# Optimization experiments

Measured on AMD Instinct MI355X. Metric: run time of the kernel, lower is better.

The kernel has to match this reference:

```python
import jax, jax.numpy as jnp
import numpy as np

CLIP_LENGTH = 256.0
NUM_CLASSES = 21
OVERLAP_THRESH = 0.5
GAMMA = 2.0
ALPHA = 0.25
EPS = float(np.finfo(np.float32).eps)

B, K, N_GT = 32, 32768, 32


def setup_inputs() -> dict:
    key = jax.random.key(0)
    ks = jax.random.split(key, 9)
    loc_data = jax.random.uniform(ks[0], (B, K, 2), jnp.float32) * 64.0 + 1.0  # frame-unit offsets
    conf_data = jax.random.normal(ks[1], (B, K, NUM_CLASSES), jnp.float32)
    prop_loc_data = jax.random.normal(ks[2], (B, K, 2), jnp.float32)
    prop_conf_data = jax.random.normal(ks[3], (B, K, NUM_CLASSES), jnp.float32)
    center_data = jax.random.normal(ks[4], (B, K, 1), jnp.float32)
    priors = jax.random.uniform(ks[5], (K, 1), jnp.float32)  # normalized centers in [0,1]
    t0 = jax.random.uniform(ks[6], (B, N_GT), jnp.float32) * 0.8
    dur = jax.random.uniform(ks[7], (B, N_GT), jnp.float32) * 0.18 + 0.02
    t1 = jnp.minimum(t0 + dur, 1.0)
    labels = jax.random.randint(ks[8], (B, N_GT), 1, NUM_CLASSES).astype(jnp.float32)
    targets = jnp.stack([t0, t1, labels], axis=-1)  # [B, N, 3]
    return {"loc_data": loc_data, "conf_data": conf_data, "prop_loc_data": prop_loc_data,
            "prop_conf_data": prop_conf_data, "center_data": center_data,
            "priors": priors, "targets": targets}


def _calc_iou(pred, target):
    pl, pr = pred[..., 0], pred[..., 1]
    tl, tr = target[..., 0], target[..., 1]
    inter = jnp.minimum(pl, tl) + jnp.minimum(pr, tr)
    union = (pl + pr) + (tl + tr) - inter
    return inter / jnp.maximum(union, EPS)


def _giou_loss(pred, target):
    pl, pr = pred[..., 0], pred[..., 1]
    tl, tr = target[..., 0], target[..., 1]
    inter = jnp.minimum(pl, tl) + jnp.minimum(pr, tr)
    union = (pl + pr) + (tl + tr) - inter
    ious = inter / jnp.maximum(union, EPS)
    ac = jnp.maximum(pl, tl) + jnp.maximum(pr, tr)
    gious = ious - (ac - union) / jnp.maximum(ac, EPS)
    return 1.0 - gious


_ALPHA_VEC = jnp.full((NUM_CLASSES,), 1.0 - ALPHA, jnp.float32).at[0].set(ALPHA)


def _focal_sum(logits, tgt):
    # FocalLoss_Ori with pre-softmax inside MultiSegmentLoss; reduction=sum
    probs = jax.nn.softmax(logits, axis=-1)
    pt = jnp.take_along_axis(probs, tgt[..., None], axis=-1)[..., 0] + 1e-10
    return (-_ALPHA_VEC[tgt] * (1.0 - pt) ** GAMMA * jnp.log(pt)).sum()


def _match_targets(loc_data_ng, priors, targets):
    # everything here mirrors the torch.no_grad() matching block
    truths = targets[..., :2]                       # [B,N,2]
    labels = targets[..., 2].astype(jnp.int32)      # [B,N]
    center = priors[:, 0]                           # [K]
    left = (center[None, :, None] - truths[:, None, :, 0]) * CLIP_LENGTH   # [B,K,N]
    right = (truths[:, None, :, 1] - center[None, :, None]) * CLIP_LENGTH  # [B,K,N]
    maxn = CLIP_LENGTH * 2.0
    area = jnp.where((left < 0) | (right < 0), maxn, left + right)
    best_area = area.min(-1)                        # [B,K]
    best_idx = area.argmin(-1)                      # [B,K]
    t0 = jnp.take_along_axis(truths[..., 0], best_idx, axis=1)
    t1 = jnp.take_along_axis(truths[..., 1], best_idx, axis=1)
    loc_t = jnp.stack([(center[None, :] - t0) * CLIP_LENGTH,
                       (t1 - center[None, :]) * CLIP_LENGTH], axis=-1)     # [B,K,2]
    conf_t = jnp.take_along_axis(labels, best_idx, axis=1)
    conf_t = jnp.where(best_area >= maxn, 0, conf_t)                       # [B,K]
    iou = _calc_iou(loc_data_ng, loc_t)
    prop_conf_t = jnp.where(iou < OVERLAP_THRESH, 0, conf_t)
    prop_w = loc_data_ng[..., 0] + loc_data_ng[..., 1]
    prop_loc_t = (loc_t - loc_data_ng) / (0.5 * prop_w[..., None])
    return loc_t, conf_t, prop_loc_t, prop_conf_t


def reference(loc_data, conf_data, prop_loc_data, prop_conf_data, center_data, priors, targets):
    loc_t, conf_t, prop_loc_t, prop_conf_t = _match_targets(
        jax.lax.stop_gradient(loc_data), priors, targets)

    pos = conf_t > 0
    posf = pos.astype(loc_data.dtype)
    N = jnp.maximum(posf.sum(), 1.0)
    prop_pos = prop_conf_t > 0
    ppf = prop_pos.astype(loc_data.dtype)
    PN = jnp.maximum(ppf.sum(), 1.0)

    # GIoU localization loss over positives
    loss_l = (_giou_loss(loc_data, loc_t) * posf).sum() / N

    # L1 proposal refinement loss over proposal positives
    loss_prop_l = (jnp.abs(prop_loc_data - prop_loc_t).sum(-1) * ppf).sum() / PN

    # centerness BCE-with-logits against refined IoU, over positives
    prop_pre_w = loc_data[..., 0:1] + loc_data[..., 1:2]
    cur_loc_p = 0.5 * prop_pre_w * prop_loc_data + loc_data
    ious_ct = jnp.maximum(_calc_iou(cur_loc_p, loc_t), 0.0)
    x = center_data[..., 0]
    bce = jnp.maximum(x, 0.0) - x * ious_ct + jnp.log1p(jnp.exp(-jnp.abs(x)))
    loss_ct = (bce * posf).sum() / N

    # focal classification losses over all anchors
    loss_c = _focal_sum(conf_data, conf_t) / N
    loss_prop_c = _focal_sum(prop_conf_data, prop_conf_t) / PN

    return (loss_l, loss_c, loss_prop_l, loss_prop_c, loss_ct)
```

## Files before the change

kernel.cpp:

```cpp
#include <hip/hip_runtime.h>
#include <math.h>

#define NCLS 21
#define NGT 32
#define CLIPLEN 256.0f
#define MAXN 512.0f
#define FEPS 1.1920928955078125e-07f

#define ROWF 21
#define WCH (64 * ROWF)


__device__ __forceinline__ void glds16(const float* g, float* l) {
    __builtin_amdgcn_global_load_lds(
        (const __attribute__((address_space(1))) void*)g,
        (__attribute__((address_space(3))) void*)l, 16, 0, 0);
}
__device__ __forceinline__ void glds4(const float* g, float* l) {
    __builtin_amdgcn_global_load_lds(
        (const __attribute__((address_space(1))) void*)g,
        (__attribute__((address_space(3))) void*)l, 4, 0, 0);
}

__device__ __forceinline__ float focal_term_lds(const float* __restrict__ row, int tgt) {
    float r[NCLS];
#pragma unroll
    for (int i = 0; i < NCLS; ++i) r[i] = row[i];
    float m = r[0];
#pragma unroll
    for (int i = 1; i < NCLS; ++i) m = fmaxf(m, r[i]);
    float s = 0.0f;
    float tl = 0.0f;
#pragma unroll
    for (int i = 0; i < NCLS; ++i) {
        s += __expf(r[i] - m);
        if (i == tgt) tl = r[i];
    }
    float lse = m + __logf(s);
    float pt = __expf(tl - lse) + 1e-10f;
    float a = (tgt == 0) ? 0.25f : 0.75f;
    float om = 1.0f - pt;
    return -a * om * om * __logf(pt);
}

template <bool PARTIALS>
__global__ __launch_bounds__(256) void msl_main(
    const float* __restrict__ loc_data,
    const float* __restrict__ conf_data,
    const float* __restrict__ prop_loc_data,
    const float* __restrict__ prop_conf_data,
    const float* __restrict__ center_data,
    const float* __restrict__ priors,
    const float* __restrict__ targets,
    double* __restrict__ ws,
    int K, int nblk)
{
    __shared__ float s_cls[2][4 * WCH];
    __shared__ float s_t0[NGT], s_t1[NGT], s_lb[NGT];
    __shared__ float s_red[7 * 4];

    const int b    = blockIdx.y;
    const int tid  = threadIdx.x;
    const int lane = tid & 63;
    const int w    = tid >> 6;
    const int kblk = blockIdx.x * 256;
    const int k    = kblk + tid;
    const size_t idx = (size_t)b * K + k;

    if (tid < NGT) {
        const float* tg = targets + ((size_t)b * NGT + tid) * 3;
        s_t0[tid] = tg[0];
        s_t1[tid] = tg[1];
        s_lb[tid] = tg[2];
    }

    {
        const size_t chunk0 = ((size_t)b * K + kblk + w * 64) * ROWF;
        const float* gc = conf_data + chunk0;
        const float* gp = prop_conf_data + chunk0;
        float* lc = &s_cls[0][w * WCH];
        float* lp = &s_cls[1][w * WCH];
#pragma unroll
        for (int i = 0; i < 5; ++i)
            glds16(gc + i * 256 + lane * 4, lc + i * 256);
        glds4(gc + 1280 + lane, lc + 1280);
#pragma unroll
        for (int i = 0; i < 5; ++i)
            glds16(gp + i * 256 + lane * 4, lp + i * 256);
        glds4(gp + 1280 + lane, lp + 1280);
    }

    const float2 loc = ((const float2*)loc_data)[idx];
    const float2 plo = ((const float2*)prop_loc_data)[idx];
    const float  x   = center_data[idx];
    const float  c   = priors[k];

    __syncthreads();

    float bestA = 3.0e38f;
    int bestN = 0;
#pragma unroll
    for (int n = 0; n < NGT; ++n) {
        float l = (c - s_t0[n]) * CLIPLEN;
        float r = (s_t1[n] - c) * CLIPLEN;
        float a = (l < 0.0f || r < 0.0f) ? MAXN : (l + r);
        if (a < bestA) { bestA = a; bestN = n; }
    }
    const float t0 = s_t0[bestN];
    const float t1 = s_t1[bestN];
    const float tl = (c - t0) * CLIPLEN;
    const float tr = (t1 - c) * CLIPLEN;
    int conf_t = (bestA >= MAXN) ? 0 : (int)s_lb[bestN];

    const float pl = loc.x, pr = loc.y;

    const float inter = fminf(pl, tl) + fminf(pr, tr);
    const float uni   = pl + pr + tl + tr - inter;
    const float iou   = inter / fmaxf(uni, FEPS);

    const int prop_conf_t = (iou < 0.5f) ? 0 : conf_t;
    const float posf = (conf_t > 0) ? 1.0f : 0.0f;
    const float ppf  = (prop_conf_t > 0) ? 1.0f : 0.0f;

    const float ac   = fmaxf(pl, tl) + fmaxf(pr, tr);
    const float giou = iou - (ac - uni) / fmaxf(ac, FEPS);
    const float v_ll = (1.0f - giou) * posf;

    const float prop_w = pl + pr;
    const float inv_hw = 1.0f / (0.5f * prop_w);
    const float plt0 = (tl - pl) * inv_hw;
    const float plt1 = (tr - pr) * inv_hw;
    const float v_lpl = (fabsf(plo.x - plt0) + fabsf(plo.y - plt1)) * ppf;

    const float cur0 = 0.5f * prop_w * plo.x + pl;
    const float cur1 = 0.5f * prop_w * plo.y + pr;
    const float in2  = fminf(cur0, tl) + fminf(cur1, tr);
    const float un2  = cur0 + cur1 + tl + tr - in2;
    const float iou2 = fmaxf(in2 / fmaxf(un2, FEPS), 0.0f);
    const float bce  = fmaxf(x, 0.0f) - x * iou2 + log1pf(__expf(-fabsf(x)));
    const float v_ct = bce * posf;

    asm volatile("s_waitcnt vmcnt(0)" ::: "memory");
    const float* rowc = &s_cls[0][w * WCH + lane * ROWF];
    const float* rowp = &s_cls[1][w * WCH + lane * ROWF];
    const float v_lc  = focal_term_lds(rowc, conf_t);
    const float v_lpc = focal_term_lds(rowp, prop_conf_t);

    float vals[7] = { v_ll, v_lc, v_lpl, v_lpc, v_ct, posf, ppf };
#pragma unroll
    for (int i = 0; i < 7; ++i) {
        float v = vals[i];
#pragma unroll
        for (int off = 32; off > 0; off >>= 1) v += __shfl_xor(v, off);
        if (lane == 0) s_red[i * 4 + w] = v;
    }
    __syncthreads();
    if (tid == 0) {
        const int blk = blockIdx.y * gridDim.x + blockIdx.x;
#pragma unroll
        for (int i = 0; i < 7; ++i) {
            double s = (double)s_red[i * 4 + 0] + (double)s_red[i * 4 + 1]
                     + (double)s_red[i * 4 + 2] + (double)s_red[i * 4 + 3];
            if (PARTIALS) ws[(size_t)i * nblk + blk] = s;
            else          atomicAdd(&ws[i], s);
        }
    }
}

__global__ __launch_bounds__(256) void msl_reduce(
    const double* __restrict__ p, int nblk, float* __restrict__ out)
{
    __shared__ double s_acc[7];
    __shared__ double s_w[4];
    const int tid  = threadIdx.x;
    const int lane = tid & 63;
    const int w    = tid >> 6;

    for (int i = 0; i < 7; ++i) {
        double v = 0.0;
        for (int j = tid; j < nblk; j += 256) v += p[(size_t)i * nblk + j];
#pragma unroll
        for (int off = 32; off > 0; off >>= 1) v += __shfl_xor(v, off);
        if (lane == 0) s_w[w] = v;
        __syncthreads();
        if (tid == 0) s_acc[i] = s_w[0] + s_w[1] + s_w[2] + s_w[3];
        __syncthreads();
    }
    if (tid == 0) {
        const double N  = fmax(s_acc[5], 1.0);
        const double PN = fmax(s_acc[6], 1.0);
        out[0] = (float)(s_acc[0] / N);
        out[1] = (float)(s_acc[1] / N);
        out[2] = (float)(s_acc[2] / PN);
        out[3] = (float)(s_acc[3] / PN);
        out[4] = (float)(s_acc[4] / N);
    }
}

__global__ void msl_finalize(const double* __restrict__ acc, float* __restrict__ out) {
    const double N  = fmax(acc[5], 1.0);
    const double PN = fmax(acc[6], 1.0);
    out[0] = (float)(acc[0] / N);
    out[1] = (float)(acc[1] / N);
    out[2] = (float)(acc[2] / PN);
    out[3] = (float)(acc[3] / PN);
    out[4] = (float)(acc[4] / N);
}

extern "C" void kernel_launch(void* const* d_in, const int* in_sizes, int n_in,
                              void* d_out, int out_size, void* d_ws, size_t ws_size,
                              hipStream_t stream) {
    const float* loc_data       = (const float*)d_in[0];
    const float* conf_data      = (const float*)d_in[1];
    const float* prop_loc_data  = (const float*)d_in[2];
    const float* prop_conf_data = (const float*)d_in[3];
    const float* center_data    = (const float*)d_in[4];
    const float* priors         = (const float*)d_in[5];
    const float* targets        = (const float*)d_in[6];
    float* out = (float*)d_out;

    const int K = in_sizes[5];
    const int B = in_sizes[6] / (NGT * 3);
    const int nblk = (K / 256) * B;

    double* ws = (double*)d_ws;
    dim3 grid(K / 256, B);

    if (ws_size >= (size_t)7 * nblk * sizeof(double)) {
        msl_main<true><<<grid, 256, 0, stream>>>(loc_data, conf_data, prop_loc_data,
                                                 prop_conf_data, center_data, priors,
                                                 targets, ws, K, nblk);
        msl_reduce<<<1, 256, 0, stream>>>(ws, nblk, out);
    } else {
        hipMemsetAsync(ws, 0, 7 * sizeof(double), stream);
        msl_main<false><<<grid, 256, 0, stream>>>(loc_data, conf_data, prop_loc_data,
                                                  prop_conf_data, center_data, priors,
                                                  targets, ws, K, nblk);
        msl_finalize<<<1, 1, 0, stream>>>(ws, out);
    }
}
```

Before: 77.36 us.

## Halve LDS staging by reusing one per-wave buffer for conf and prop_conf rows

```diff
diff --git a/kernel.cpp b/kernel.cpp
--- a/kernel.cpp
+++ b/kernel.cpp
@@ -22,10 +22,19 @@
         (__attribute__((address_space(3))) void*)l, 4, 0, 0);
 }
 
-__device__ __forceinline__ float focal_term_lds(const float* __restrict__ row, int tgt) {
-    float r[NCLS];
+__device__ __forceinline__ void stage_rows(const float* g, float* l, int lane) {
+#pragma unroll
+    for (int i = 0; i < 5; ++i)
+        glds16(g + i * 256 + lane * 4, l + i * 256);
+    glds4(g + 1280 + lane, l + 1280);
+}
+
+__device__ __forceinline__ void load_row(const float* __restrict__ row, float* r) {
 #pragma unroll
     for (int i = 0; i < NCLS; ++i) r[i] = row[i];
+}
+
+__device__ __forceinline__ float focal_from_regs(const float* r, int tgt) {
     float m = r[0];
 #pragma unroll
     for (int i = 1; i < NCLS; ++i) m = fmaxf(m, r[i]);
@@ -44,7 +53,7 @@
 }
 
 template <bool PARTIALS>
-__global__ __launch_bounds__(256) void msl_main(
+__global__ __launch_bounds__(256, 7) void msl_main(
     const float* __restrict__ loc_data,
     const float* __restrict__ conf_data,
     const float* __restrict__ prop_loc_data,
@@ -55,7 +64,7 @@
     double* __restrict__ ws,
     int K, int nblk)
 {
-    __shared__ float s_cls[2][4 * WCH];
+    __shared__ float s_cls[4][WCH];
     __shared__ float s_t0[NGT], s_t1[NGT], s_lb[NGT];
     __shared__ float s_red[7 * 4];
 
@@ -74,21 +83,10 @@
         s_lb[tid] = tg[2];
     }
 
-    {
-        const size_t chunk0 = ((size_t)b * K + kblk + w * 64) * ROWF;
-        const float* gc = conf_data + chunk0;
-        const float* gp = prop_conf_data + chunk0;
-        float* lc = &s_cls[0][w * WCH];
-        float* lp = &s_cls[1][w * WCH];
-#pragma unroll
-        for (int i = 0; i < 5; ++i)
-            glds16(gc + i * 256 + lane * 4, lc + i * 256);
-        glds4(gc + 1280 + lane, lc + 1280);
-#pragma unroll
-        for (int i = 0; i < 5; ++i)
-            glds16(gp + i * 256 + lane * 4, lp + i * 256);
-        glds4(gp + 1280 + lane, lp + 1280);
-    }
+    const size_t chunk0 = ((size_t)b * K + kblk + w * 64) * ROWF;
+    float* lbuf = &s_cls[w][0];
+
+    stage_rows(conf_data + chunk0, lbuf, lane);
 
     const float2 loc = ((const float2*)loc_data)[idx];
     const float2 plo = ((const float2*)prop_loc_data)[idx];
@@ -141,10 +139,21 @@
     const float v_ct = bce * posf;
 
     asm volatile("s_waitcnt vmcnt(0)" ::: "memory");
-    const float* rowc = &s_cls[0][w * WCH + lane * ROWF];
-    const float* rowp = &s_cls[1][w * WCH + lane * ROWF];
-    const float v_lc  = focal_term_lds(rowc, conf_t);
-    const float v_lpc = focal_term_lds(rowp, prop_conf_t);
+    __builtin_amdgcn_sched_barrier(0);
+    const float* rowp = lbuf + lane * ROWF;
+    float rr[NCLS];
+    load_row(rowp, rr);
+    asm volatile("s_waitcnt lgkmcnt(0)" ::: "memory");
+    __builtin_amdgcn_sched_barrier(0);
+
+    stage_rows(prop_conf_data + chunk0, lbuf, lane);
+
+    const float v_lc = focal_from_regs(rr, conf_t);
+
+    asm volatile("s_waitcnt vmcnt(0)" ::: "memory");
+    __builtin_amdgcn_sched_barrier(0);
+    load_row(rowp, rr);
+    const float v_lpc = focal_from_regs(rr, prop_conf_t);
 
     float vals[7] = { v_ll, v_lc, v_lpl, v_lpc, v_ct, posf, ppf };
 #pragma unroll
```

New measurement: 72.60 us. 6.2% less time.
